# Kernel optimization log

Hardware: AMD Instinct MI355X
Metric: run time of the kernel (lower is better)

Reference implementation:

```python
import jax, jax.numpy as jnp
import numpy as np

KSIZE = 3
RES_SCALE = 0.2
WITH_RESIDUAL = True


def setup_inputs() -> dict:
    key = jax.random.key(0)
    x = jax.random.normal(key, (8, 3, 1024, 1024), dtype=jnp.float32)
    return {"x": x}


def reference(x) -> jnp.ndarray:
    B, C, H, W = x.shape
    k = KSIZE
    p = k // 2
    # zero padding matches F.unfold(padding=k//2)
    xp = jnp.pad(x, ((0, 0), (0, 0), (p, p), (p, p)))
    # [B, C, k*k, H, W] stack of shifted views (k*k = 9, small static loop)
    patches = jnp.stack(
        [xp[:, :, di:di + H, dj:dj + W] for di in range(k) for dj in range(k)],
        axis=2,
    )
    # median of odd-sized window = middle element of sorted values
    med = jnp.sort(patches, axis=2)[:, :, (k * k) // 2]
    if WITH_RESIDUAL:
        return x + RES_SCALE * (med - x)
    return med
```

## Files before the change

kernel.cpp:

```cpp
#include <hip/hip_runtime.h>


#define S2(a, b) { float _t = fminf(a, b); b = fmaxf(a, b); a = _t; }

__device__ __forceinline__ float med3f(float a, float b, float c) {
    return fmaxf(fminf(a, b), fminf(fmaxf(a, b), c));
}

constexpr int ROWS = 16;

struct Row { float v[6]; };

__global__ __launch_bounds__(256, 4) void median_blur_kernel(
    const float* __restrict__ xin, float* __restrict__ out)
{
    const int W = 1024, H = 1024;
    const int tx = threadIdx.x;
    const int x0 = tx << 2;
    const int y0 = blockIdx.x * ROWS;
    const size_t plane = (size_t)blockIdx.y * H * W;
    const float* base  = xin + plane;
    float*       obase = out + plane;

    const int  xl = (x0 > 0)     ? x0 - 1 : 0;
    const int  xr = (x0 + 4 < W) ? x0 + 4 : W - 1;
    const bool lz = (x0 == 0);
    const bool rz = (x0 + 4 >= W);

    auto load_row = [&](int y, Row& d) {
        if ((unsigned)y < (unsigned)H) {
            const float* row = base + (size_t)y * W;
            const float4 c = *reinterpret_cast<const float4*>(row + x0);
            const float  l = row[xl];
            const float  r = row[xr];
            d.v[0] = lz ? 0.0f : l;
            d.v[1] = c.x; d.v[2] = c.y; d.v[3] = c.z; d.v[4] = c.w;
            d.v[5] = rz ? 0.0f : r;
        } else {
#pragma unroll
            for (int j = 0; j < 6; ++j) d.v[j] = 0.0f;
        }
    };

    Row t, m, b, p0, p1;
    load_row(y0 - 1, t);
    load_row(y0,     m);
    load_row(y0 + 1, b);
    load_row(y0 + 2, p0);
    load_row(y0 + 3, p1);

#pragma unroll
    for (int r = 0; r < ROWS; ++r) {
        Row nx;
        {
            const int yn = (r <= ROWS - 4) ? (y0 + r + 4) : H;
            load_row(yn, nx);
        }

        float lo[6], mi[6], hi[6];
#pragma unroll
        for (int j = 0; j < 6; ++j) {
            float a = t.v[j], c0 = m.v[j], d = b.v[j];
            S2(a, c0); S2(c0, d); S2(a, c0);
            lo[j] = a; mi[j] = c0; hi[j] = d;
        }

        float4 o; float* op = &o.x;
#pragma unroll
        for (int j = 0; j < 4; ++j) {
            float mxlo = fmaxf(lo[j], fmaxf(lo[j + 1], lo[j + 2]));
            float mnhi = fminf(hi[j], fminf(hi[j + 1], hi[j + 2]));
            float mdmi = med3f(mi[j], mi[j + 1], mi[j + 2]);
            float med  = med3f(mxlo, mdmi, mnhi);
            float xc   = m.v[j + 1];
            op[j] = xc + 0.2f * (med - xc);
        }
        *reinterpret_cast<float4*>(obase + (size_t)(y0 + r) * W + x0) = o;

        t = m; m = b; b = p0; p0 = p1; p1 = nx;
    }
}

extern "C" void kernel_launch(void* const* d_in, const int* in_sizes, int n_in,
                              void* d_out, int out_size, void* d_ws, size_t ws_size,
                              hipStream_t stream) {
    const float* x = (const float*)d_in[0];
    float* out = (float*)d_out;
    const int H = 1024, W = 1024;
    const int planes = in_sizes[0] / (H * W);
    dim3 block(256);
    dim3 grid(H / ROWS, planes);
    median_blur_kernel<<<grid, block, 0, stream>>>(x, out);
}
```

Before: 182.3 us.

## Stream rows via async global-to-LDS ring buffer with nontemporal stores

Replaces per-thread register loads of halo rows with asynchronous global_load_lds copies into a 6-row shared-memory ring, prefetched five rows ahead and synchronized by vmcnt waits plus block barriers. Neighbor columns are then read from LDS instead of issuing extra unaligned global loads. Output uses nontemporal stores to avoid cache pollution. It adds per-row barriers and LDS traffic and drops the occupancy hint, trading that for deeper memory-latency hiding.

```diff
diff --git a/kernel.cpp b/kernel.cpp
--- a/kernel.cpp
+++ b/kernel.cpp
@@ -1,20 +1,21 @@
 #include <hip/hip_runtime.h>
 
 
-#define S2(a, b) { float _t = fminf(a, b); b = fmaxf(a, b); a = _t; }
+typedef float v4f __attribute__((ext_vector_type(4)));
 
-__device__ __forceinline__ float med3f(float a, float b, float c) {
-    return fmaxf(fminf(a, b), fminf(fmaxf(a, b), c));
+#define S2(a,b) { float _t=fminf(a,b); (b)=fmaxf(a,b); (a)=_t; }
+__device__ __forceinline__ float med3f(float a,float b,float c){
+    return fmaxf(fminf(a,b), fminf(fmaxf(a,b),c));
 }
 
+constexpr int W = 1024, H = 1024;
 constexpr int ROWS = 16;
+constexpr int NBUF = 6;
 
-struct Row { float v[6]; };
-
-__global__ __launch_bounds__(256, 4) void median_blur_kernel(
+__global__ __launch_bounds__(256) void median_blur_kernel(
     const float* __restrict__ xin, float* __restrict__ out)
 {
-    const int W = 1024, H = 1024;
+    __shared__ float smem[NBUF * W];
     const int tx = threadIdx.x;
     const int x0 = tx << 2;
     const int y0 = blockIdx.x * ROWS;
@@ -22,63 +23,75 @@
     const float* base  = xin + plane;
     float*       obase = out + plane;
 
-    const int  xl = (x0 > 0)     ? x0 - 1 : 0;
-    const int  xr = (x0 + 4 < W) ? x0 + 4 : W - 1;
-    const bool lz = (x0 == 0);
-    const bool rz = (x0 + 4 >= W);
+    const int  il = (x0 > 0)     ? x0 - 1 : 0;
+    const int  ir = (x0 + 4 < W) ? x0 + 4 : W - 1;
+    const bool lz = (x0 == 0), rz = (x0 + 4 >= W);
 
-    auto load_row = [&](int y, Row& d) {
-        if ((unsigned)y < (unsigned)H) {
-            const float* row = base + (size_t)y * W;
-            const float4 c = *reinterpret_cast<const float4*>(row + x0);
-            const float  l = row[xl];
-            const float  r = row[xr];
-            d.v[0] = lz ? 0.0f : l;
-            d.v[1] = c.x; d.v[2] = c.y; d.v[3] = c.z; d.v[4] = c.w;
-            d.v[5] = rz ? 0.0f : r;
+    auto issue = [&](int s) {
+        int y = y0 - 1 + s;
+        y = y < 0 ? 0 : (y > H - 1 ? H - 1 : y);
+        const float* g = base + (size_t)y * W + x0;
+        float* l = &smem[(s % NBUF) * W + x0];
+        __builtin_amdgcn_global_load_lds(
+            (const __attribute__((address_space(1))) void*)g,
+            (__attribute__((address_space(3))) void*)l, 16, 0, 0);
+    };
+
+    issue(0); issue(1); issue(2); issue(3); issue(4);
+
+    auto readrow = [&](int s, bool valid, float* d) {
+        if (valid) {
+            const float* sm = &smem[(s % NBUF) * W];
+            v4f c = *reinterpret_cast<const v4f*>(sm + x0);
+            float l = sm[il], r = sm[ir];
+            d[0] = lz ? 0.0f : l;
+            d[1] = c.x; d[2] = c.y; d[3] = c.z; d[4] = c.w;
+            d[5] = rz ? 0.0f : r;
         } else {
 #pragma unroll
-            for (int j = 0; j < 6; ++j) d.v[j] = 0.0f;
+            for (int j = 0; j < 6; ++j) d[j] = 0.0f;
         }
     };
 
-    Row t, m, b, p0, p1;
-    load_row(y0 - 1, t);
-    load_row(y0,     m);
-    load_row(y0 + 1, b);
-    load_row(y0 + 2, p0);
-    load_row(y0 + 3, p1);
-
-#pragma unroll
-    for (int r = 0; r < ROWS; ++r) {
-        Row nx;
-        {
-            const int yn = (r <= ROWS - 4) ? (y0 + r + 4) : H;
-            load_row(yn, nx);
-        }
-
+    auto compute_store = [&](int r, const float* t, const float* m, const float* b) {
         float lo[6], mi[6], hi[6];
 #pragma unroll
         for (int j = 0; j < 6; ++j) {
-            float a = t.v[j], c0 = m.v[j], d = b.v[j];
+            float a = t[j], c0 = m[j], d = b[j];
             S2(a, c0); S2(c0, d); S2(a, c0);
             lo[j] = a; mi[j] = c0; hi[j] = d;
         }
-
-        float4 o; float* op = &o.x;
+        v4f o;
 #pragma unroll
         for (int j = 0; j < 4; ++j) {
             float mxlo = fmaxf(lo[j], fmaxf(lo[j + 1], lo[j + 2]));
             float mnhi = fminf(hi[j], fminf(hi[j + 1], hi[j + 2]));
             float mdmi = med3f(mi[j], mi[j + 1], mi[j + 2]);
             float med  = med3f(mxlo, mdmi, mnhi);
-            float xc   = m.v[j + 1];
-            op[j] = xc + 0.2f * (med - xc);
+            float xc   = m[j + 1];
+            o[j] = xc + 0.2f * (med - xc);
         }
-        *reinterpret_cast<float4*>(obase + (size_t)(y0 + r) * W + x0) = o;
+        __builtin_nontemporal_store(o, (v4f*)(obase + (size_t)(y0 + r) * W + x0));
+    };
 
-        t = m; m = b; b = p0; p0 = p1; p1 = nx;
-    }
+#define ITER(R, VM) {                                                   \
+    asm volatile("" ::: "memory");                                      \
+    __builtin_amdgcn_s_waitcnt(0xF70 | (VM));                           \
+    __builtin_amdgcn_s_barrier();                                       \
+    asm volatile("" ::: "memory");                                      \
+    float t[6], mm[6], bb[6];                                           \
+    readrow((R),     y0 + (R) - 1 >= 0, t);                             \
+    readrow((R) + 1, true,              mm);                            \
+    readrow((R) + 2, y0 + (R) + 1 < H,  bb);                            \
+    if ((R) + 5 <= ROWS + 1) issue((R) + 5);                            \
+    compute_store((R), t, mm, bb);                                      \
+}
+
+    ITER(0, 2)  ITER(1, 2)  ITER(2, 2)  ITER(3, 2)
+    ITER(4, 2)  ITER(5, 2)  ITER(6, 2)  ITER(7, 2)
+    ITER(8, 2)  ITER(9, 2)  ITER(10, 2) ITER(11, 2)
+    ITER(12, 2) ITER(13, 2) ITER(14, 1) ITER(15, 0)
+#undef ITER
 }
 
 extern "C" void kernel_launch(void* const* d_in, const int* in_sizes, int n_in,
@@ -86,7 +99,6 @@
                               hipStream_t stream) {
     const float* x = (const float*)d_in[0];
     float* out = (float*)d_out;
-    const int H = 1024, W = 1024;
     const int planes = in_sizes[0] / (H * W);
     dim3 block(256);
     dim3 grid(H / ROWS, planes);
```

Result: no change. 180.6 us (-0.9%).
